# Kernel tuning notes

Hardware: AMD Instinct MI355X
Metric: run time of the kernel (lower is better)

The kernel has to match this reference:

```python
import jax, jax.numpy as jnp
import numpy as np

SPATIAL = 128   # N: wall spatial resolution
CROP = 256      # M: temporal bins (power of 2)
BIN_LEN = 0.01
WALL_SIZE = 2.0


def _grids():
    # Reproduces parpareparam(): normalized freq-domain coordinate grids, [2M,2N,2N].
    M, N = CROP, SPATIAL
    width = WALL_SIZE / 2.0
    trange = CROP * BIN_LEN  # crop * c * (bin_len / c)
    zdim = (np.arange(2 * M, dtype=np.float32) - M) / M
    xdim = (np.arange(2 * N, dtype=np.float32) - N) / N
    gz = np.ascontiguousarray(np.broadcast_to(zdim[:, None, None], (2 * M, 2 * N, 2 * N)))
    gy = np.ascontiguousarray(np.broadcast_to(xdim[None, :, None], (2 * M, 2 * N, 2 * N)))
    gx = np.ascontiguousarray(np.broadcast_to(xdim[None, None, :], (2 * M, 2 * N, 2 * N)))
    fkrange = (N * trange / (M * width * 4.0)) ** 2
    gznew = np.sqrt(fkrange * (gx ** 2 + gy ** 2) + gz ** 2).astype(np.float32)
    return jnp.asarray(gx), jnp.asarray(gy), jnp.asarray(gz), jnp.asarray(gznew)


def _grid_sample_3d(vol, x, y, z):
    """Trilinear grid sample, padding_mode='zeros', align_corners=False.
    vol: [B, D, H, W] (complex ok); x/y/z: [Dg,Hg,Wg] in [-1,1] (x->W, y->H, z->D)."""
    B, D, H, W = vol.shape
    ix = ((x + 1.0) * W - 1.0) * 0.5
    iy = ((y + 1.0) * H - 1.0) * 0.5
    iz = ((z + 1.0) * D - 1.0) * 0.5
    ix0 = jnp.floor(ix); iy0 = jnp.floor(iy); iz0 = jnp.floor(iz)
    fx = ix - ix0; fy = iy - iy0; fz = iz - iz0
    ix0 = ix0.astype(jnp.int32); iy0 = iy0.astype(jnp.int32); iz0 = iz0.astype(jnp.int32)
    out = jnp.zeros((B,) + x.shape, vol.dtype)
    for dz in (0, 1):
        for dy in (0, 1):
            for dx in (0, 1):
                xi = ix0 + dx; yi = iy0 + dy; zi = iz0 + dz
                valid = (xi >= 0) & (xi < W) & (yi >= 0) & (yi < H) & (zi >= 0) & (zi < D)
                w = ((fx if dx else 1.0 - fx) * (fy if dy else 1.0 - fy) * (fz if dz else 1.0 - fz))
                w = jnp.where(valid, w, 0.0)
                xi = jnp.clip(xi, 0, W - 1); yi = jnp.clip(yi, 0, H - 1); zi = jnp.clip(zi, 0, D - 1)
                out = out + vol[:, zi, yi, xi] * w  # gather 8 trilinear corners
    return out


def _fk_forward(feat_padded):
    # feat_padded: [B, Dn, CROP, N, N] float32
    B, Dn, T, H, W = feat_padded.shape
    M, N = CROP, SPATIAL
    gx, gy, gz, gznew = _grids()
    gridz = jnp.arange(M, dtype=jnp.float32) / (M - 1)  # gridz_1xMx1x1
    data = feat_padded.reshape(B * Dn, M, N, N) * (gridz ** 2)[None, :, None, None]
    data = jax.nn.relu(data)
    # sqrt with grad-safe double-where (torch sqrt backward at 0 is nan; math limit here is 0)
    data = jnp.where(data > 0, jnp.sqrt(jnp.where(data > 0, data, 1.0)), 0.0)
    pad = jnp.zeros((B * Dn, 2 * M, 2 * N, 2 * N), jnp.float32).at[:, :M, :N, :N].set(data)
    fre = jnp.fft.fftn(pad, axes=(1, 2, 3))            # torch.rfft(x,3,onesided=False)
    fre = jnp.roll(fre, (M, N, N), axis=(1, 2, 3))      # fftshift rolls
    t = _grid_sample_3d(fre, gx, gy, gznew)             # Stolt frequency resampling
    t = t.at[:, :M + 1].set(0.0)                        # z0pos = M+1 (first zdim>0)
    t = t * (jnp.abs(gz) / (gznew + 1e-8))[None]        # |f_z| Jacobian scaling
    t = jnp.roll(t, (M, N, N), axis=(1, 2, 3))          # ifftshift (even dims)
    vol = jnp.fft.ifftn(t, axes=(1, 2, 3))[:, :M, :N, :N]
    out = vol.real ** 2 + vol.imag ** 2                 # squared magnitude
    return out.reshape(B, Dn, M, N, N)


def setup_inputs() -> dict:
    key = jax.random.key(0)
    feat = jax.random.uniform(key, (1, 1, CROP, SPATIAL, SPATIAL), dtype=jnp.float32)
    return {"feture_bxdxtxhxw": feat, "tbes": 0, "tens": CROP}


def reference(feture_bxdxtxhxw, tbes, tens):
    tbe, ten = int(tbes), int(tens)
    featpad = jnp.pad(feture_bxdxtxhxw, ((0, 0), (0, 0), (tbe, CROP - ten), (0, 0), (0, 0)))
    return _fk_forward(featpad)
```

## Files before the change

kernel.cpp:

```cpp
#include <hip/hip_runtime.h>


typedef float __attribute__((ext_vector_type(2))) cpx;

__device__ float4 g_tw4[512];

__device__ __forceinline__ cpx cswap(cpx a){ return __builtin_shufflevector(a, a, 1, 0); }
__device__ __forceinline__ cpx cmji(cpx a){ return cswap(a)*(cpx){1.0f, -1.0f}; }
__device__ __forceinline__ cpx cmpi(cpx a){ return cswap(a)*(cpx){-1.0f, 1.0f}; }

__device__ __forceinline__ int rev4_8(int k){
    return ((k & 3) << 6) | ((k & 12) << 2) | ((k >> 2) & 12) | (k >> 6);
}

__global__ void k_tw(){
    int j = threadIdx.x;
    double a = -2.0*3.14159265358979323846*(double)j/512.0;
    float c = (float)cos(a), s = (float)sin(a);
    g_tw4[j] = make_float4(c, c, -s, s);
}

template<bool INV>
__device__ __forceinline__ cpx twmul(cpx a, int k){
    float4 t = g_tw4[k & 511];
    cpx wl = {t.x, t.y};
    cpx wh = {t.z, t.w};
    cpx r = a*wl;
    return INV ? (r - cswap(a)*wh) : (r + cswap(a)*wh);
}

template<bool INV>
__device__ __forceinline__ void dft4(cpx* x){
    cpx e0 = x[0] + x[2], e1 = x[0] - x[2];
    cpx o0 = x[1] + x[3], o1 = x[1] - x[3];
    x[0] = e0 + o0;
    x[2] = e0 - o0;
    cpx j1 = INV ? cmpi(o1) : cmji(o1);
    x[1] = e1 + j1;
    x[3] = e1 - j1;
}

template<bool INV>
__device__ __forceinline__ void dft4_h2(cpx* x){
    cpx a0 = x[0], a1 = x[1];
    x[0] = a0 + a1;
    x[2] = a0 - a1;
    cpx j1 = INV ? cmpi(a1) : cmji(a1);
    x[1] = a0 + j1;
    x[3] = a0 - j1;
}

template<bool INV>
__device__ __forceinline__ void dft4_lo2(cpx* x){
    cpx e0 = x[0] + x[2], e1 = x[0] - x[2];
    cpx o0 = x[1] + x[3], o1 = x[1] - x[3];
    x[0] = e0 + o0;
    x[1] = e1 + (INV ? cmpi(o1) : cmji(o1));
}

template<bool INV>
__device__ __forceinline__ void dft8(cpx* x){
    const float s = 0.70710678118654752440f;
    cpx e0 = x[0] + x[4], e2 = x[0] - x[4];
    cpx e1 = x[2] + x[6], e3 = x[2] - x[6];
    cpx E0 = e0 + e1, E2 = e0 - e1;
    cpx j3 = INV ? cmpi(e3) : cmji(e3);
    cpx E1 = e2 + j3, E3 = e2 - j3;
    cpx o0 = x[1] + x[5], o2 = x[1] - x[5];
    cpx o1 = x[3] + x[7], o3 = x[3] - x[7];
    cpx O0 = o0 + o1, O2 = o0 - o1;
    cpx k3 = INV ? cmpi(o3) : cmji(o3);
    cpx O1 = o2 + k3, O3 = o2 - k3;
    cpx W1, W2, W3;
    if (!INV){
        W1 = s*(O1 + cmji(O1));
        W2 = cmji(O2);
        W3 = s*(cmji(O3) - O3);
    } else {
        W1 = s*(O1 + cmpi(O1));
        W2 = cmpi(O2);
        W3 = s*(cmpi(O3) - O3);
    }
    x[0] = E0 + O0; x[4] = E0 - O0;
    x[1] = E1 + W1; x[5] = E1 - W1;
    x[2] = E2 + W2; x[6] = E2 - W2;
    x[3] = E3 + W3; x[7] = E3 - W3;
}

template<bool INV>
__device__ __forceinline__ void dft8_h4(cpx* x){
    const float s = 0.70710678118654752440f;
    cpx a0 = x[0], a1 = x[1], a2 = x[2], a3 = x[3];
    cpx E0 = a0 + a2, E2 = a0 - a2;
    cpx j3 = INV ? cmpi(a2) : cmji(a2);
    cpx E1 = a0 + j3, E3 = a0 - j3;
    cpx O0 = a1 + a3, O2 = a1 - a3;
    cpx k3 = INV ? cmpi(a3) : cmji(a3);
    cpx O1 = a1 + k3, O3 = a1 - k3;
    cpx W1, W2, W3;
    if (!INV){
        W1 = s*(O1 + cmji(O1));
        W2 = cmji(O2);
        W3 = s*(cmji(O3) - O3);
    } else {
        W1 = s*(O1 + cmpi(O1));
        W2 = cmpi(O2);
        W3 = s*(cmpi(O3) - O3);
    }
    x[0] = E0 + O0; x[4] = E0 - O0;
    x[1] = E1 + W1; x[5] = E1 - W1;
    x[2] = E2 + W2; x[6] = E2 - W2;
    x[3] = E3 + W3; x[7] = E3 - W3;
}

template<bool INV>
__device__ __forceinline__ void dft8_lo4(cpx* x){
    const float s = 0.70710678118654752440f;
    cpx e0 = x[0] + x[4], e2 = x[0] - x[4];
    cpx e1 = x[2] + x[6], e3 = x[2] - x[6];
    cpx E0 = e0 + e1, E2 = e0 - e1;
    cpx j3 = INV ? cmpi(e3) : cmji(e3);
    cpx E1 = e2 + j3, E3 = e2 - j3;
    cpx o0 = x[1] + x[5], o2 = x[1] - x[5];
    cpx o1 = x[3] + x[7], o3 = x[3] - x[7];
    cpx O0 = o0 + o1, O2 = o0 - o1;
    cpx k3 = INV ? cmpi(o3) : cmji(o3);
    cpx O1 = o2 + k3, O3 = o2 - k3;
    cpx W1, W2, W3;
    if (!INV){
        W1 = s*(O1 + cmji(O1));
        W2 = cmji(O2);
        W3 = s*(cmji(O3) - O3);
    } else {
        W1 = s*(O1 + cmpi(O1));
        W2 = cmpi(O2);
        W3 = s*(cmpi(O3) - O3);
    }
    x[0] = E0 + O0;
    x[1] = E1 + W1;
    x[2] = E2 + W2;
    x[3] = E3 + W3;
}

template<bool INV, bool CROP>
__device__ __forceinline__ void fft256_r4_tail(cpx* sl, int b){
    cpx x[4];
    {
        int j = b & 15, g = (b >> 4) << 6;
        #pragma unroll
        for (int t = 0; t < 4; ++t) x[t] = sl[g + j + (t << 4)];
        dft4<INV>(x);
        #pragma unroll
        for (int r = 1; r < 4; ++r) x[r] = twmul<INV>(x[r], 8*j*r);
        #pragma unroll
        for (int r = 0; r < 4; ++r) sl[g + j + (r << 4)] = x[r];
    }
    __syncthreads();
    {
        int j = b & 3, g = (b >> 2) << 4;
        #pragma unroll
        for (int t = 0; t < 4; ++t) x[t] = sl[g + j + (t << 2)];
        dft4<INV>(x);
        #pragma unroll
        for (int r = 1; r < 4; ++r) x[r] = twmul<INV>(x[r], 32*j*r);
        #pragma unroll
        for (int r = 0; r < 4; ++r) sl[g + j + (r << 2)] = x[r];
    }
    __syncthreads();
    {
        int g = b << 2;
        #pragma unroll
        for (int t = 0; t < 4; ++t) x[t] = sl[g + t];
        if (CROP){
            dft4_lo2<INV>(x);
            sl[g] = x[0]; sl[g + 1] = x[1];
        } else {
            dft4<INV>(x);
            #pragma unroll
            for (int r = 0; r < 4; ++r) sl[g + r] = x[r];
        }
    }
    __syncthreads();
}

__global__ __launch_bounds__(256) void k_fft_x_fill(const float* __restrict__ feat, cpx* __restrict__ V){
    __shared__ cpx s[4*256];
    int tid = threadIdx.x;
    int line0 = blockIdx.x << 2;
    int l = tid >> 6, b = tid & 63;
    int line = line0 + l;
    cpx* sl = s + l*256;
    {
        int z = line >> 7;
        float g = (float)z*(1.0f/255.0f);
        const float* fl = feat + ((size_t)line << 7);
        float a  = fl[b]*g*g;       a  = a  > 0.0f ? sqrtf(a)  : 0.0f;
        float bb = fl[b + 64]*g*g;  bb = bb > 0.0f ? sqrtf(bb) : 0.0f;
        cpx x[4];
        x[0] = (cpx){a, 0.0f};
        x[1] = (cpx){bb, 0.0f};
        dft4_h2<false>(x);
        #pragma unroll
        for (int r = 1; r < 4; ++r) x[r] = twmul<false>(x[r], 2*b*r);
        #pragma unroll
        for (int r = 0; r < 4; ++r) sl[b + (r << 6)] = x[r];
    }
    __syncthreads();
    fft256_r4_tail<false, false>(sl, b);
    for (int i = tid; i < 4*128; i += 256){
        int ll = i >> 7, f4 = i & 127;
        int lin = line0 + ll;
        int base = ((lin >> 7) << 16) + ((lin & 127) << 8);
        const cpx* sll = s + ll*256;
        int e0 = 2*f4;
        cpx Fm = e0 ? sll[rev4_8(e0 - 1) ^ 2] : (cpx){0.0f, 0.0f};
        cpx F0 = sll[rev4_8(e0) ^ 2];
        cpx F1 = sll[rev4_8(e0 + 1) ^ 2];
        cpx o0 = 0.5f*(Fm + F0);
        cpx o1 = 0.5f*(F0 + F1);
        float4 o = make_float4(o0.x, o0.y, o1.x, o1.y);
        ((float4*)(V + base))[f4] = o;
    }
}

__global__ __launch_bounds__(256) void k_fft_x_inv_mag(const cpx* __restrict__ W,
                                                       float* __restrict__ out){
    __shared__ cpx s[4*256];
    int tid = threadIdx.x;
    int line0 = blockIdx.x << 2;
    int l = tid >> 6, b = tid & 63;
    int line = line0 + l;
    int base = ((line >> 7) << 16) + ((line & 127) << 8);
    cpx* sl = s + l*256;
    {
        cpx x[4];
        #pragma unroll
        for (int t = 0; t < 4; ++t) x[t] = W[base + b + (t << 6)];
        dft4<true>(x);
        #pragma unroll
        for (int r = 1; r < 4; ++r) x[r] = twmul<true>(x[r], 2*b*r);
        #pragma unroll
        for (int r = 0; r < 4; ++r) sl[b + (r << 6)] = x[r];
    }
    __syncthreads();
    fft256_r4_tail<true, true>(sl, b);
    {
        int z = line >> 7, y = line & 127;
        cpx v0 = sl[rev4_8(2*b)];
        cpx v1 = sl[rev4_8(2*b + 1)];
        const float SC2 = (1.0f/33554432.0f)*(1.0f/33554432.0f);
        float2 o = make_float2((v0.x*v0.x + v0.y*v0.y)*SC2,
                               (v1.x*v1.x + v1.y*v1.y)*SC2);
        ((float2*)(out + (((size_t)(z*128 + y)) << 7)))[b] = o;
    }
}

template<bool INV, bool HALF_IN, bool HALF_OUT>
__global__ __launch_bounds__(1024) void k_fft_y(cpx* __restrict__ V){
    __shared__ cpx s[256*16];
    int tid = threadIdx.x;
    int z  = blockIdx.x >> 4;
    int x0 = (blockIdx.x & 15) << 4;
    int base = (z << 16) + x0;
    int c = tid & 15, idx = tid >> 4;
    cpx x[4];
    {
        int j = idx;
        if (HALF_IN){
            x[0] = V[base + (j << 8) + c];
            x[1] = V[base + ((j + 64) << 8) + c];
            dft4_h2<INV>(x);
        } else {
            #pragma unroll
            for (int t = 0; t < 4; ++t) x[t] = V[base + ((j + (t << 6)) << 8) + c];
            dft4<INV>(x);
        }
        #pragma unroll
        for (int r = 1; r < 4; ++r) x[r] = twmul<INV>(x[r], 2*j*r);
        #pragma unroll
        for (int r = 0; r < 4; ++r) s[(j + (r << 6))*16 + c] = x[r];
    }
    __syncthreads();
    {
        int j = idx & 15, g = (idx >> 4) << 6;
        #pragma unroll
        for (int t = 0; t < 4; ++t) x[t] = s[(g + j + (t << 4))*16 + c];
        dft4<INV>(x);
        #pragma unroll
        for (int r = 1; r < 4; ++r) x[r] = twmul<INV>(x[r], 8*j*r);
        #pragma unroll
        for (int r = 0; r < 4; ++r) s[(g + j + (r << 4))*16 + c] = x[r];
    }
    __syncthreads();
    {
        int j = idx & 3, g = (idx >> 2) << 4;
        #pragma unroll
        for (int t = 0; t < 4; ++t) x[t] = s[(g + j + (t << 2))*16 + c];
        dft4<INV>(x);
        #pragma unroll
        for (int r = 1; r < 4; ++r) x[r] = twmul<INV>(x[r], 32*j*r);
        #pragma unroll
        for (int r = 0; r < 4; ++r) s[(g + j + (r << 2))*16 + c] = x[r];
    }
    __syncthreads();
    {
        int g = idx << 2;
        #pragma unroll
        for (int t = 0; t < 4; ++t) x[t] = s[(g + t)*16 + c];
        if (HALF_OUT){
            dft4_lo2<INV>(x);
            s[g*16 + c] = x[0]; s[(g + 1)*16 + c] = x[1];
        } else {
            dft4<INV>(x);
            #pragma unroll
            for (int r = 0; r < 4; ++r) s[(g + r)*16 + c] = x[r];
        }
    }
    __syncthreads();
    const int YOUT = HALF_OUT ? 128 : 256;
    for (int i = tid; i < YOUT*8; i += 1024){
        int f4c = i & 7, e = i >> 3;
        if (!INV){
            int p0 = rev4_8(e) ^ 2;
            float4 S0 = ((const float4*)(s + p0*16))[f4c];
            float4 S1 = make_float4(0.0f, 0.0f, 0.0f, 0.0f);
            if (e){
                int p1 = rev4_8(e - 1) ^ 2;
                S1 = ((const float4*)(s + p1*16))[f4c];
            }
            float4 o;
            o.x = 0.5f*(S0.x + S1.x); o.y = 0.5f*(S0.y + S1.y);
            o.z = 0.5f*(S0.z + S1.z); o.w = 0.5f*(S0.w + S1.w);
            ((float4*)(V + base + (e << 8)))[f4c] = o;
        } else {
            int p = rev4_8(e);
            ((float4*)(V + base + (e << 8)))[f4c] = ((const float4*)(s + p*16))[f4c];
        }
    }
}

__global__ __launch_bounds__(1024) void k_fft_z_fwd(cpx* __restrict__ V){
    __shared__ cpx s[512*16];
    int tid = threadIdx.x;
    int y  = blockIdx.x >> 4;
    int x0 = (blockIdx.x & 15) << 4;
    int base = (y << 8) + x0;
    int c = tid & 15, idx = tid >> 4;
    cpx x[8];
    {
        int j = idx;
        #pragma unroll
        for (int t = 0; t < 4; ++t)
            x[t] = V[base + (((size_t)(j + (t << 6))) << 16) + c];
        dft8_h4<false>(x);
        #pragma unroll
        for (int r = 1; r < 8; ++r) x[r] = twmul<false>(x[r], j*r);
        #pragma unroll
        for (int r = 0; r < 8; ++r) s[(j + (r << 6))*16 + c] = x[r];
    }
    __syncthreads();
    {
        int j = idx & 7, g = (idx >> 3) << 6;
        #pragma unroll
        for (int t = 0; t < 8; ++t) x[t] = s[(g + j + (t << 3))*16 + c];
        dft8<false>(x);
        #pragma unroll
        for (int r = 1; r < 8; ++r) x[r] = twmul<false>(x[r], 8*j*r);
        #pragma unroll
        for (int r = 0; r < 8; ++r) s[(g + j + (r << 3))*16 + c] = x[r];
    }
    __syncthreads();
    {
        int g = idx << 3;
        #pragma unroll
        for (int t = 0; t < 8; ++t) x[t] = s[(g + t)*16 + c];
        dft8_lo4<false>(x);
        #pragma unroll
        for (int r = 0; r < 4; ++r) s[(g + r)*16 + c] = x[r];
    }
    __syncthreads();
    for (int i = tid; i < 256*8; i += 1024){
        int f4c = i & 7, e = i >> 3;
        int p = ((e & 7) << 6) | (e & 56) | (e >> 6);
        ((float4*)(V + base + ((e + 256) << 16)))[f4c] = ((const float4*)(s + p*16))[f4c];
    }
}

__device__ __forceinline__ cpx zgather_g(const cpx* __restrict__ Vsrc, int zd, float rxy, int srcoff){
    if (!zd) return (cpx){0.0f, 0.0f};
    float gz = (float)zd*(1.0f/256.0f);
    float gzn = sqrtf(rxy + gz*gz);
    float iz = ((gzn + 1.0f)*512.0f - 1.0f)*0.5f;
    float fiz = floorf(iz);
    int iz0 = (int)fiz;
    float fz = iz - fiz;
    float sc = gz/(gzn + 1e-8f);
    int z0 = iz0 < 511 ? iz0 : 511;
    int z1 = (iz0 + 1) < 511 ? (iz0 + 1) : 511;
    float w0 = (iz0     <= 511) ? (1.0f - fz)*sc : 0.0f;
    float w1 = (iz0 + 1 <= 511) ? fz*sc : 0.0f;
    cpx a = Vsrc[((size_t)z0 << 16) + srcoff];
    cpx b = Vsrc[((size_t)z1 << 16) + srcoff];
    return a*w0 + b*w1;
}

__global__ __launch_bounds__(1024) void k_stolt_fftz_inv(const cpx* __restrict__ Vsrc, cpx* __restrict__ V){
    __shared__ cpx s[512*16];
    int tid = threadIdx.x;
    int y  = blockIdx.x >> 4;
    int x0 = (blockIdx.x & 15) << 4;
    int base = (y << 8) + x0;
    int c = tid & 15, idx = tid >> 4;
    int xs = ((x0 + c) + 128) & 255;
    int ys = (y + 128) & 255;
    float gx = (float)(xs - 128)*(1.0f/128.0f);
    float gy = (float)(ys - 128)*(1.0f/128.0f);
    float rxy = 0.1024f*(gx*gx + gy*gy);
    int srcoff = (ys << 8) + xs;
    cpx x[8];
    {
        int j = idx;
        #pragma unroll
        for (int t = 0; t < 4; ++t)
            x[t] = zgather_g(Vsrc, j + (t << 6), rxy, srcoff);
        dft8_h4<true>(x);
        #pragma unroll
        for (int r = 1; r < 8; ++r) x[r] = twmul<true>(x[r], j*r);
        #pragma unroll
        for (int r = 0; r < 8; ++r) s[(j + (r << 6))*16 + c] = x[r];
    }
    __syncthreads();
    {
        int j = idx & 7, g = (idx >> 3) << 6;
        #pragma unroll
        for (int t = 0; t < 8; ++t) x[t] = s[(g + j + (t << 3))*16 + c];
        dft8<true>(x);
        #pragma unroll
        for (int r = 1; r < 8; ++r) x[r] = twmul<true>(x[r], 8*j*r);
        #pragma unroll
        for (int r = 0; r < 8; ++r) s[(g + j + (r << 3))*16 + c] = x[r];
    }
    __syncthreads();
    {
        int g = idx << 3;
        #pragma unroll
        for (int t = 0; t < 8; ++t) x[t] = s[(g + t)*16 + c];
        dft8_lo4<true>(x);
        #pragma unroll
        for (int r = 0; r < 4; ++r) s[(g + r)*16 + c] = x[r];
    }
    __syncthreads();
    for (int i = tid; i < 256*8; i += 1024){
        int f4c = i & 7, e = i >> 3;
        int p = ((e & 7) << 6) | (e & 56) | (e >> 6);
        ((float4*)(V + base + (e << 16)))[f4c] = ((const float4*)(s + p*16))[f4c];
    }
}

extern "C" void kernel_launch(void* const* d_in, const int* in_sizes, int n_in,
                              void* d_out, int out_size, void* d_ws, size_t ws_size,
                              hipStream_t stream){
    const float* feat = (const float*)d_in[0];
    float* out = (float*)d_out;

    const size_t WS_NEED = (size_t)512*256*256*8;
    if (ws_size < WS_NEED){
        hipMemsetAsync(d_out, 0, (size_t)out_size*sizeof(float), stream);
        return;
    }
    cpx* V = (cpx*)d_ws;

    k_tw<<<1, 512, 0, stream>>>();
    k_fft_x_fill<<<8192, 256, 0, stream>>>(feat, V);
    k_fft_y<false, true, false><<<4096, 1024, 0, stream>>>(V);
    k_fft_z_fwd<<<4096, 1024, 0, stream>>>(V);
    k_stolt_fftz_inv<<<4096, 1024, 0, stream>>>(V, V);
    k_fft_y<true, false, true><<<4096, 1024, 0, stream>>>(V);
    k_fft_x_inv_mag<<<8192, 256, 0, stream>>>(V, out);
}
```

Measured before the change: 264.4 us.

## Fuse forward z-FFT, Stolt resampling and inverse z-FFT into one kernel

Merges the forward z-FFT and the Stolt-resample plus inverse z-FFT kernels into a single kernel. Each block keeps the forward z spectrum of its column tile in shared memory and does the z interpolation from there instead of round-tripping through global memory. The inverse-y half-output path also writes its results straight from registers, skipping a shared-memory stage and a barrier. This cuts a full volume write and gather-read pass, at the cost of extra barriers, heavier shared-memory reuse and less coalesced direct stores.

```diff
diff --git a/kernel.cpp b/kernel.cpp
--- a/kernel.cpp
+++ b/kernel.cpp
@@ -11,6 +11,9 @@
 
 __device__ __forceinline__ int rev4_8(int k){
     return ((k & 3) << 6) | ((k & 12) << 2) | ((k >> 2) & 12) | (k >> 6);
+}
+__device__ __forceinline__ int rev8_9(int k){
+    return ((k & 7) << 6) | (k & 56) | (k >> 6);
 }
 
 __global__ void k_tw(){
@@ -303,55 +306,57 @@
         for (int r = 0; r < 4; ++r) s[(g + j + (r << 2))*16 + c] = x[r];
     }
     __syncthreads();
-    {
+    if (HALF_OUT){
         int g = idx << 2;
         #pragma unroll
         for (int t = 0; t < 4; ++t) x[t] = s[(g + t)*16 + c];
-        if (HALF_OUT){
-            dft4_lo2<INV>(x);
-            s[g*16 + c] = x[0]; s[(g + 1)*16 + c] = x[1];
-        } else {
-            dft4<INV>(x);
-            #pragma unroll
-            for (int r = 0; r < 4; ++r) s[(g + r)*16 + c] = x[r];
-        }
-    }
-    __syncthreads();
-    const int YOUT = HALF_OUT ? 128 : 256;
-    for (int i = tid; i < YOUT*8; i += 1024){
+        dft4_lo2<INV>(x);
+        int e0 = rev4_8(g);
+        V[base + (e0 << 8) + c] = x[0];
+        V[base + ((e0 + 64) << 8) + c] = x[1];
+        return;
+    }
+    {
+        int g = idx << 2;
+        #pragma unroll
+        for (int t = 0; t < 4; ++t) x[t] = s[(g + t)*16 + c];
+        dft4<INV>(x);
+        #pragma unroll
+        for (int r = 0; r < 4; ++r) s[(g + r)*16 + c] = x[r];
+    }
+    __syncthreads();
+    for (int i = tid; i < 256*8; i += 1024){
         int f4c = i & 7, e = i >> 3;
-        if (!INV){
-            int p0 = rev4_8(e) ^ 2;
-            float4 S0 = ((const float4*)(s + p0*16))[f4c];
-            float4 S1 = make_float4(0.0f, 0.0f, 0.0f, 0.0f);
-            if (e){
-                int p1 = rev4_8(e - 1) ^ 2;
-                S1 = ((const float4*)(s + p1*16))[f4c];
-            }
-            float4 o;
-            o.x = 0.5f*(S0.x + S1.x); o.y = 0.5f*(S0.y + S1.y);
-            o.z = 0.5f*(S0.z + S1.z); o.w = 0.5f*(S0.w + S1.w);
-            ((float4*)(V + base + (e << 8)))[f4c] = o;
-        } else {
-            int p = rev4_8(e);
-            ((float4*)(V + base + (e << 8)))[f4c] = ((const float4*)(s + p*16))[f4c];
-        }
-    }
-}
-
-__global__ __launch_bounds__(1024) void k_fft_z_fwd(cpx* __restrict__ V){
+        int p0 = rev4_8(e) ^ 2;
+        float4 S0 = ((const float4*)(s + p0*16))[f4c];
+        float4 S1 = make_float4(0.0f, 0.0f, 0.0f, 0.0f);
+        if (e){
+            int p1 = rev4_8(e - 1) ^ 2;
+            S1 = ((const float4*)(s + p1*16))[f4c];
+        }
+        float4 o;
+        o.x = 0.5f*(S0.x + S1.x); o.y = 0.5f*(S0.y + S1.y);
+        o.z = 0.5f*(S0.z + S1.z); o.w = 0.5f*(S0.w + S1.w);
+        ((float4*)(V + base + (e << 8)))[f4c] = o;
+    }
+}
+
+__global__ __launch_bounds__(1024, 8) void k_fftz_fused(cpx* __restrict__ V){
     __shared__ cpx s[512*16];
     int tid = threadIdx.x;
-    int y  = blockIdx.x >> 4;
-    int x0 = (blockIdx.x & 15) << 4;
-    int base = (y << 8) + x0;
+    int yD  = blockIdx.x >> 4;
+    int x0D = (blockIdx.x & 15) << 4;
+    int baseD = (yD << 8) + x0D;
+    int yS  = (yD + 128) & 255;
+    int x0S = (x0D + 128) & 255;
+    int baseS = (yS << 8) + x0S;
     int c = tid & 15, idx = tid >> 4;
     cpx x[8];
-    {
-        int j = idx;
+    int j = idx;
+    {
         #pragma unroll
         for (int t = 0; t < 4; ++t)
-            x[t] = V[base + (((size_t)(j + (t << 6))) << 16) + c];
+            x[t] = V[baseS + (((size_t)(j + (t << 6))) << 16) + c];
         dft8_h4<false>(x);
         #pragma unroll
         for (int r = 1; r < 8; ++r) x[r] = twmul<false>(x[r], j*r);
@@ -360,14 +365,14 @@
     }
     __syncthreads();
     {
-        int j = idx & 7, g = (idx >> 3) << 6;
-        #pragma unroll
-        for (int t = 0; t < 8; ++t) x[t] = s[(g + j + (t << 3))*16 + c];
+        int jj = idx & 7, g = (idx >> 3) << 6;
+        #pragma unroll
+        for (int t = 0; t < 8; ++t) x[t] = s[(g + jj + (t << 3))*16 + c];
         dft8<false>(x);
         #pragma unroll
-        for (int r = 1; r < 8; ++r) x[r] = twmul<false>(x[r], 8*j*r);
-        #pragma unroll
-        for (int r = 0; r < 8; ++r) s[(g + j + (r << 3))*16 + c] = x[r];
+        for (int r = 1; r < 8; ++r) x[r] = twmul<false>(x[r], 8*jj*r);
+        #pragma unroll
+        for (int r = 0; r < 8; ++r) s[(g + jj + (r << 3))*16 + c] = x[r];
     }
     __syncthreads();
     {
@@ -376,69 +381,58 @@
         for (int t = 0; t < 8; ++t) x[t] = s[(g + t)*16 + c];
         dft8_lo4<false>(x);
         #pragma unroll
-        for (int r = 0; r < 4; ++r) s[(g + r)*16 + c] = x[r];
-    }
-    __syncthreads();
-    for (int i = tid; i < 256*8; i += 1024){
-        int f4c = i & 7, e = i >> 3;
-        int p = ((e & 7) << 6) | (e & 56) | (e >> 6);
-        ((float4*)(V + base + ((e + 256) << 16)))[f4c] = ((const float4*)(s + p*16))[f4c];
-    }
-}
-
-__device__ __forceinline__ cpx zgather_g(const cpx* __restrict__ Vsrc, int zd, float rxy, int srcoff){
-    if (!zd) return (cpx){0.0f, 0.0f};
-    float gz = (float)zd*(1.0f/256.0f);
-    float gzn = sqrtf(rxy + gz*gz);
-    float iz = ((gzn + 1.0f)*512.0f - 1.0f)*0.5f;
-    float fiz = floorf(iz);
-    int iz0 = (int)fiz;
-    float fz = iz - fiz;
-    float sc = gz/(gzn + 1e-8f);
-    int z0 = iz0 < 511 ? iz0 : 511;
-    int z1 = (iz0 + 1) < 511 ? (iz0 + 1) : 511;
-    float w0 = (iz0     <= 511) ? (1.0f - fz)*sc : 0.0f;
-    float w1 = (iz0 + 1 <= 511) ? fz*sc : 0.0f;
-    cpx a = Vsrc[((size_t)z0 << 16) + srcoff];
-    cpx b = Vsrc[((size_t)z1 << 16) + srcoff];
-    return a*w0 + b*w1;
-}
-
-__global__ __launch_bounds__(1024) void k_stolt_fftz_inv(const cpx* __restrict__ Vsrc, cpx* __restrict__ V){
-    __shared__ cpx s[512*16];
-    int tid = threadIdx.x;
-    int y  = blockIdx.x >> 4;
-    int x0 = (blockIdx.x & 15) << 4;
-    int base = (y << 8) + x0;
-    int c = tid & 15, idx = tid >> 4;
-    int xs = ((x0 + c) + 128) & 255;
-    int ys = (y + 128) & 255;
-    float gx = (float)(xs - 128)*(1.0f/128.0f);
-    float gy = (float)(ys - 128)*(1.0f/128.0f);
-    float rxy = 0.1024f*(gx*gx + gy*gy);
-    int srcoff = (ys << 8) + xs;
-    cpx x[8];
-    {
-        int j = idx;
-        #pragma unroll
-        for (int t = 0; t < 4; ++t)
-            x[t] = zgather_g(Vsrc, j + (t << 6), rxy, srcoff);
+        for (int r = 0; r < 4; ++r){
+            int e = (r << 6) | ((idx & 7) << 3) | (idx >> 3);
+            s[e*16 + c] = x[r];
+        }
+    }
+    __syncthreads();
+    {
+        int xs = x0S + c;
+        float gx = (float)(xs - 128)*(1.0f/128.0f);
+        float gy = (float)(yS - 128)*(1.0f/128.0f);
+        float rxy = 0.1024f*(gx*gx + gy*gy);
+        #pragma unroll
+        for (int t = 0; t < 4; ++t){
+            int zd = j + (t << 6);
+            cpx r = (cpx){0.0f, 0.0f};
+            if (zd){
+                float gz = (float)zd*(1.0f/256.0f);
+                float gzn = sqrtf(rxy + gz*gz);
+                float iz = ((gzn + 1.0f)*512.0f - 1.0f)*0.5f;
+                float fiz = floorf(iz);
+                int iz0 = (int)fiz;
+                float fz = iz - fiz;
+                float sc = gz/(gzn + 1e-8f);
+                int b0 = (iz0 < 511 ? iz0 : 511) - 256;
+                int b1 = ((iz0 + 1) < 511 ? (iz0 + 1) : 511) - 256;
+                float w0 = (iz0     <= 511) ? (1.0f - fz)*sc : 0.0f;
+                float w1 = (iz0 + 1 <= 511) ? fz*sc : 0.0f;
+                cpx a = s[(b0 << 4) + c];
+                cpx b = s[(b1 << 4) + c];
+                r = a*w0 + b*w1;
+            }
+            x[t] = r;
+        }
         dft8_h4<true>(x);
         #pragma unroll
         for (int r = 1; r < 8; ++r) x[r] = twmul<true>(x[r], j*r);
+    }
+    __syncthreads();
+    {
         #pragma unroll
         for (int r = 0; r < 8; ++r) s[(j + (r << 6))*16 + c] = x[r];
     }
     __syncthreads();
     {
-        int j = idx & 7, g = (idx >> 3) << 6;
-        #pragma unroll
-        for (int t = 0; t < 8; ++t) x[t] = s[(g + j + (t << 3))*16 + c];
+        int jj = idx & 7, g = (idx >> 3) << 6;
+        #pragma unroll
+        for (int t = 0; t < 8; ++t) x[t] = s[(g + jj + (t << 3))*16 + c];
         dft8<true>(x);
         #pragma unroll
-        for (int r = 1; r < 8; ++r) x[r] = twmul<true>(x[r], 8*j*r);
-        #pragma unroll
-        for (int r = 0; r < 8; ++r) s[(g + j + (r << 3))*16 + c] = x[r];
+        for (int r = 1; r < 8; ++r) x[r] = twmul<true>(x[r], 8*jj*r);
+        #pragma unroll
+        for (int r = 0; r < 8; ++r) s[(g + jj + (r << 3))*16 + c] = x[r];
     }
     __syncthreads();
     {
@@ -447,13 +441,10 @@
         for (int t = 0; t < 8; ++t) x[t] = s[(g + t)*16 + c];
         dft8_lo4<true>(x);
         #pragma unroll
-        for (int r = 0; r < 4; ++r) s[(g + r)*16 + c] = x[r];
-    }
-    __syncthreads();
-    for (int i = tid; i < 256*8; i += 1024){
-        int f4c = i & 7, e = i >> 3;
-        int p = ((e & 7) << 6) | (e & 56) | (e >> 6);
-        ((float4*)(V + base + (e << 16)))[f4c] = ((const float4*)(s + p*16))[f4c];
+        for (int r = 0; r < 4; ++r){
+            int e = (r << 6) | ((idx & 7) << 3) | (idx >> 3);
+            V[baseD + (((size_t)(e + 256)) << 16) + c] = x[r];
+        }
     }
 }
 
@@ -468,13 +459,13 @@
         hipMemsetAsync(d_out, 0, (size_t)out_size*sizeof(float), stream);
         return;
     }
-    cpx* V = (cpx*)d_ws;
+    cpx* V  = (cpx*)d_ws;
+    cpx* Vu = V + (size_t)256*65536;
 
     k_tw<<<1, 512, 0, stream>>>();
     k_fft_x_fill<<<8192, 256, 0, stream>>>(feat, V);
     k_fft_y<false, true, false><<<4096, 1024, 0, stream>>>(V);
-    k_fft_z_fwd<<<4096, 1024, 0, stream>>>(V);
-    k_stolt_fftz_inv<<<4096, 1024, 0, stream>>>(V, V);
-    k_fft_y<true, false, true><<<4096, 1024, 0, stream>>>(V);
-    k_fft_x_inv_mag<<<8192, 256, 0, stream>>>(V, out);
-}
+    k_fftz_fused<<<4096, 1024, 0, stream>>>(V);
+    k_fft_y<true, false, true><<<4096, 1024, 0, stream>>>(Vu);
+    k_fft_x_inv_mag<<<8192, 256, 0, stream>>>(Vu, out);
+}
```

Measured after the change: 258.6 us. 2.2% less time.
